# Performance work log

Hardware: AMD Instinct MI355X
Metric: run time of the kernel (lower is better)

The kernel has to match this reference:

```python
import jax, jax.numpy as jnp
import numpy as np

N_NODES = 10000


def gcn_conv(x, W, b, src, dst, num_nodes):
    # PyG GCNConv (eval): h = x @ W; add self-loops; symmetric norm D^-1/2 A D^-1/2; sum-aggregate; + bias
    h = x @ W  # [N, out]
    loop = jnp.arange(num_nodes, dtype=src.dtype)
    s = jnp.concatenate([src, loop])  # [E+N]
    d = jnp.concatenate([dst, loop])
    deg = jax.ops.segment_sum(jnp.ones_like(d, dtype=h.dtype), d, num_segments=num_nodes)
    dinv = jnp.where(deg > 0, jax.lax.rsqrt(deg), 0.0)
    norm = dinv[s] * dinv[d]  # [E+N]
    msg = h[s] * norm[:, None]  # gather + scale
    out = jax.ops.segment_sum(msg, d, num_segments=num_nodes)  # scatter-add to dst
    return out + b


def setup_inputs() -> dict:
    key = jax.random.key(0)
    k1, k2, k3, k4 = jax.random.split(key, 4)
    in_c, hid_c, out_c = 512, 512, 256
    x = jax.random.normal(k1, (N_NODES, in_c), dtype=jnp.float32)
    edge_index = jax.random.randint(k2, (2, 160000), 0, N_NODES, dtype=jnp.int64)
    W1 = jax.random.normal(k3, (in_c, hid_c), dtype=jnp.float32) * (1.0 / np.sqrt(in_c))
    b1 = jnp.zeros((hid_c,), dtype=jnp.float32)
    W2 = jax.random.normal(k4, (hid_c, out_c), dtype=jnp.float32) * (1.0 / np.sqrt(hid_c))
    b2 = jnp.zeros((out_c,), dtype=jnp.float32)
    return {"x": x, "edge_index": edge_index, "W1": W1, "b1": b1, "W2": W2, "b2": b2}


def reference(x, edge_index, W1, b1, W2, b2):
    src, dst = edge_index[0], edge_index[1]
    h = gcn_conv(x, W1, b1, src, dst, N_NODES)
    h = jax.nn.relu(h)
    # dropout(p=0.5) is identity in eval mode
    z = gcn_conv(h, W2, b2, src, dst, N_NODES)
    return z
```

## Files before the change

### kernel.cpp

```cpp
#include <hip/hip_runtime.h>

#define NN   10000

typedef float f32x4 __attribute__((ext_vector_type(4)));
typedef short s16x8 __attribute__((ext_vector_type(8)));
typedef short s16x4 __attribute__((ext_vector_type(4)));

__device__ __forceinline__ unsigned int f2bf(float f) {
  unsigned int u = __float_as_uint(f);
  return (u + 0x7fffu + ((u >> 16) & 1u)) >> 16;
}
__device__ __forceinline__ float bf2f(unsigned int h) {
  return __uint_as_float(h << 16);
}

__global__ void k_zero_int(int* __restrict__ p, int n) {
  int i = blockIdx.x * blockDim.x + threadIdx.x;
  if (i < n) p[i] = 0;
}

__global__ void k_count(const int* __restrict__ dst, int E, int* __restrict__ cnt) {
  int i = blockIdx.x * blockDim.x + threadIdx.x;
  if (i < E) atomicAdd(&cnt[dst[i]], 1);
}

__global__ __launch_bounds__(256) void k_scan(const int* __restrict__ cnt, int n,
                                              int* __restrict__ offs, float* __restrict__ dinv) {
  __shared__ int part[256];
  int t = threadIdx.x;
  int chunk = (n + 255) / 256;
  int lo = t * chunk, hi = min(lo + chunk, n);
  int s = 0;
  for (int i = lo; i < hi; ++i) s += cnt[i];
  part[t] = s;
  __syncthreads();
  for (int d = 1; d < 256; d <<= 1) {
    int v = (t >= d) ? part[t - d] : 0;
    __syncthreads();
    part[t] += v;
    __syncthreads();
  }
  int run = (t == 0) ? 0 : part[t - 1];
  for (int i = lo; i < hi; ++i) {
    offs[i] = run;
    int c = cnt[i];
    run += c;
    dinv[i] = rsqrtf((float)(c + 1));
  }
  if (t == 255) offs[n] = run;
}

__global__ void k_fill(const int* __restrict__ src, const int* __restrict__ dst, int E,
                       const int* __restrict__ offs, int* __restrict__ cur, int* __restrict__ csr) {
  int i = blockIdx.x * blockDim.x + threadIdx.x;
  if (i < E) {
    int d = dst[i];
    int p = atomicAdd(&cur[d], 1);
    csr[offs[d] + p] = src[i];
  }
}

__global__ void k_convw(const float* __restrict__ W, unsigned short* __restrict__ WT, int N) {
  int i = blockIdx.x * blockDim.x + threadIdx.x;
  if (i >= 512 * N) return;
  int k = i / N, n = i - k * N;
  float f = W[i];
  unsigned int hb = f2bf(f);
  WT[(size_t)n * 1024 + k] = (unsigned short)hb;
  WT[(size_t)n * 1024 + 512 + k] = (unsigned short)f2bf(f - bf2f(hb));
}

template <bool ASPLIT>
__global__ __launch_bounds__(256) void k_gemm_mfma(
    const void* __restrict__ Ap, const unsigned short* __restrict__ WT,
    unsigned short* __restrict__ C, int M, int N, int NTN) {
  __shared__ short Wh[64 * 40], Wl[64 * 40], Ahs[64 * 40];
  __shared__ short Als[ASPLIT ? 64 * 40 : 8];

  int nwg = gridDim.x;
  int q = nwg >> 3, r = nwg & 7;
  int xcd = blockIdx.x & 7, idx = blockIdx.x >> 3;
  int swz = (xcd < r ? xcd * (q + 1) : r * (q + 1) + (xcd - r) * q) + idx;
  int bn = (swz % NTN) * 64;
  int bm = (swz / NTN) * 64;

  int t = threadIdx.x;
  int wid = t >> 6, lane = t & 63;
  int wn = wid & 1, wm = wid >> 1;
  int lr = lane & 15, lg = lane >> 4;

  int wrow = t >> 2, kg8 = (t & 3) * 8;
  int arow = t >> 3, kc4 = (t & 7) * 4;
  int brow = t >> 2, kb8 = (t & 3) * 8;

  f32x4 acc[2][2];
  #pragma unroll
  for (int i = 0; i < 2; ++i)
    #pragma unroll
    for (int j = 0; j < 2; ++j) acc[i][j] = (f32x4){0.f, 0.f, 0.f, 0.f};

  const unsigned short* wbase = WT + (size_t)(bn + wrow) * 1024;

  for (int kk = 0; kk < 512; kk += 32) {
    __syncthreads();
    *(s16x8*)&Wh[wrow * 40 + kg8] = *(const s16x8*)&wbase[kk + kg8];
    *(s16x8*)&Wl[wrow * 40 + kg8] = *(const s16x8*)&wbase[512 + kk + kg8];
    if (ASPLIT) {
      const float* A = (const float*)Ap;
      #pragma unroll
      for (int p = 0; p < 2; ++p) {
        int row = arow + p * 32;
        int grow = bm + row;
        float4 v = make_float4(0.f, 0.f, 0.f, 0.f);
        if (grow < M) v = *(const float4*)&A[(size_t)grow * 512 + kk + kc4];
        float fs[4] = {v.x, v.y, v.z, v.w};
        s16x4 hv, lv;
        #pragma unroll
        for (int j = 0; j < 4; ++j) {
          unsigned int hb = f2bf(fs[j]);
          hv[j] = (short)hb;
          lv[j] = (short)f2bf(fs[j] - bf2f(hb));
        }
        *(s16x4*)&Ahs[row * 40 + kc4] = hv;
        *(s16x4*)&Als[row * 40 + kc4] = lv;
      }
    } else {
      const unsigned short* Ab = (const unsigned short*)Ap;
      int grow = bm + brow;
      s16x8 v = (s16x8){0, 0, 0, 0, 0, 0, 0, 0};
      if (grow < M) v = *(const s16x8*)&Ab[(size_t)grow * 512 + kk + kb8];
      *(s16x8*)&Ahs[brow * 40 + kb8] = v;
    }
    __syncthreads();

    s16x8 fwh[2], fwl[2], fah[2], fal[2];
    #pragma unroll
    for (int i = 0; i < 2; ++i) {
      int nr = wn * 32 + i * 16 + lr;
      int mr = wm * 32 + i * 16 + lr;
      fwh[i] = *(const s16x8*)&Wh[nr * 40 + lg * 8];
      fwl[i] = *(const s16x8*)&Wl[nr * 40 + lg * 8];
      fah[i] = *(const s16x8*)&Ahs[mr * 40 + lg * 8];
      if (ASPLIT) fal[i] = *(const s16x8*)&Als[mr * 40 + lg * 8];
    }
    #pragma unroll
    for (int mi = 0; mi < 2; ++mi)
      #pragma unroll
      for (int ni = 0; ni < 2; ++ni) {
        acc[mi][ni] = __builtin_amdgcn_mfma_f32_16x16x32_bf16(fwh[ni], fah[mi], acc[mi][ni], 0, 0, 0);
        acc[mi][ni] = __builtin_amdgcn_mfma_f32_16x16x32_bf16(fwl[ni], fah[mi], acc[mi][ni], 0, 0, 0);
        if (ASPLIT)
          acc[mi][ni] = __builtin_amdgcn_mfma_f32_16x16x32_bf16(fwh[ni], fal[mi], acc[mi][ni], 0, 0, 0);
      }
  }

  #pragma unroll
  for (int mi = 0; mi < 2; ++mi) {
    int m = bm + wm * 32 + mi * 16 + lr;
    if (m < M) {
      #pragma unroll
      for (int ni = 0; ni < 2; ++ni) {
        int n0 = bn + wn * 32 + ni * 16 + lg * 4;
        ushort4 cv;
        cv.x = (unsigned short)f2bf(acc[mi][ni][0]);
        cv.y = (unsigned short)f2bf(acc[mi][ni][1]);
        cv.z = (unsigned short)f2bf(acc[mi][ni][2]);
        cv.w = (unsigned short)f2bf(acc[mi][ni][3]);
        *(ushort4*)&C[(size_t)m * N + n0] = cv;
      }
    }
  }
}

template <int F, bool RELU, bool OUTBF16>
__global__ __launch_bounds__(256) void k_agg_bf(
    const unsigned short* __restrict__ H, const float* __restrict__ dinv,
    const int* __restrict__ offs, const int* __restrict__ csr,
    const float* __restrict__ bias, void* __restrict__ outp) {
  constexpr int FT = F / 8;
  constexpr int EG = 256 / FT;
  __shared__ float red[256][8];
  int node = blockIdx.x;
  int t = threadIdx.x;
  int fc = t % FT;
  int eg = t / FT;
  int lo = offs[node], hi = offs[node + 1];
  float a[8];
  #pragma unroll
  for (int j = 0; j < 8; ++j) a[j] = 0.f;
  for (int e = lo + eg; e < hi; e += EG) {
    int s = csr[e];
    float w = dinv[s];
    s16x8 v = *(const s16x8*)&H[(size_t)s * F + fc * 8];
    #pragma unroll
    for (int j = 0; j < 8; ++j) a[j] += w * bf2f((unsigned short)v[j]);
  }
  #pragma unroll
  for (int j = 0; j < 8; ++j) red[t][j] = a[j];
  __syncthreads();
  if (eg == 0) {
    #pragma unroll
    for (int g = 1; g < EG; ++g)
      #pragma unroll
      for (int j = 0; j < 8; ++j) a[j] += red[g * FT + fc][j];
    float wd = dinv[node];
    s16x8 sv = *(const s16x8*)&H[(size_t)node * F + fc * 8];
    float o[8];
    #pragma unroll
    for (int j = 0; j < 8; ++j) {
      o[j] = wd * (a[j] + wd * bf2f((unsigned short)sv[j])) + bias[fc * 8 + j];
      if (RELU) o[j] = fmaxf(o[j], 0.f);
    }
    if (OUTBF16) {
      s16x8 hv;
      #pragma unroll
      for (int j = 0; j < 8; ++j) hv[j] = (short)f2bf(o[j]);
      *(s16x8*)&((unsigned short*)outp)[(size_t)node * F + fc * 8] = hv;
    } else {
      float* op = (float*)outp;
      *(float4*)&op[(size_t)node * F + fc * 8]     = make_float4(o[0], o[1], o[2], o[3]);
      *(float4*)&op[(size_t)node * F + fc * 8 + 4] = make_float4(o[4], o[5], o[6], o[7]);
    }
  }
}

extern "C" void kernel_launch(void* const* d_in, const int* in_sizes, int n_in,
                              void* d_out, int out_size, void* d_ws, size_t ws_size,
                              hipStream_t stream) {
  (void)n_in; (void)out_size; (void)ws_size;
  const float* x  = (const float*)d_in[0];
  const int*   ei = (const int*)d_in[1];
  const float* W1 = (const float*)d_in[2];
  const float* b1 = (const float*)d_in[3];
  const float* W2 = (const float*)d_in[4];
  const float* b2 = (const float*)d_in[5];
  float* out = (float*)d_out;

  int E = in_sizes[1] / 2;
  const int* src = ei;
  const int* dst = ei + E;

  char* w = (char*)d_ws;
  float*          dinv = (float*)(w);
  int*            cnt  = (int*)(w + 65536);
  int*            cur  = (int*)(w + 131072);
  int*            offs = (int*)(w + 196608);
  int*            csr  = (int*)(w + 262144);
  unsigned short* WT1  = (unsigned short*)(w + 1048576);
  unsigned short* WT2  = (unsigned short*)(w + 2097152);
  unsigned short* h1   = (unsigned short*)(w + 3145728);
  unsigned short* a1   = (unsigned short*)(w + 14680064);
  unsigned short* h2   = (unsigned short*)(w + 26214400);

  k_zero_int<<<(NN + 255) / 256, 256, 0, stream>>>(cnt, NN);
  k_zero_int<<<(NN + 255) / 256, 256, 0, stream>>>(cur, NN);
  k_count<<<(E + 255) / 256, 256, 0, stream>>>(dst, E, cnt);
  k_scan<<<1, 256, 0, stream>>>(cnt, NN, offs, dinv);
  k_fill<<<(E + 255) / 256, 256, 0, stream>>>(src, dst, E, offs, cur, csr);

  k_convw<<<(512 * 512 + 255) / 256, 256, 0, stream>>>(W1, WT1, 512);
  k_convw<<<(512 * 256 + 255) / 256, 256, 0, stream>>>(W2, WT2, 256);

  int ntm = (NN + 63) / 64;
  k_gemm_mfma<true><<<8 * ntm, 256, 0, stream>>>(x, WT1, h1, NN, 512, 8);
  k_agg_bf<512, true, true><<<NN, 256, 0, stream>>>(h1, dinv, offs, csr, b1, a1);
  k_gemm_mfma<false><<<4 * ntm, 256, 0, stream>>>(a1, WT2, h2, NN, 256, 4);
  k_agg_bf<256, false, false><<<NN, 256, 0, stream>>>(h2, dinv, offs, csr, b2, out);
}
```

Baseline: 219.4 us.

## Enlarge GEMM M-tile to 128 rows and merge small setup kernels

The GEMM block tile grows from 64x64 to 128x64, so each wave computes 64 rows with four M fragments and reuses each loaded W fragment across twice as many MFMAs. This halves the number of workgroups and cuts repeated W staging traffic. Separately, the two zeroing kernels and the two weight-conversion kernels are each merged into one launch to save launch overhead. The larger tile raises register and LDS use and leaves fewer blocks, which may lower occupancy.

```diff
diff --git a/kernel.cpp b/kernel.cpp
--- a/kernel.cpp
+++ b/kernel.cpp
@@ -14,9 +14,9 @@
   return __uint_as_float(h << 16);
 }
 
-__global__ void k_zero_int(int* __restrict__ p, int n) {
-  int i = blockIdx.x * blockDim.x + threadIdx.x;
-  if (i < n) p[i] = 0;
+__global__ void k_zero2(int* __restrict__ p0, int* __restrict__ p1, int n) {
+  int i = blockIdx.x * blockDim.x + threadIdx.x;
+  if (i < n) { p0[i] = 0; p1[i] = 0; }
 }
 
 __global__ void k_count(const int* __restrict__ dst, int E, int* __restrict__ cnt) {
@@ -60,29 +60,38 @@
   }
 }
 
-__global__ void k_convw(const float* __restrict__ W, unsigned short* __restrict__ WT, int N) {
-  int i = blockIdx.x * blockDim.x + threadIdx.x;
-  if (i >= 512 * N) return;
-  int k = i / N, n = i - k * N;
-  float f = W[i];
-  unsigned int hb = f2bf(f);
-  WT[(size_t)n * 1024 + k] = (unsigned short)hb;
-  WT[(size_t)n * 1024 + 512 + k] = (unsigned short)f2bf(f - bf2f(hb));
+__global__ void k_convw2(const float* __restrict__ W1, unsigned short* __restrict__ WT1,
+                         const float* __restrict__ W2, unsigned short* __restrict__ WT2) {
+  int i = blockIdx.x * blockDim.x + threadIdx.x;
+  if (i < 512 * 512) {
+    int k = i >> 9, n = i & 511;
+    float f = W1[i];
+    unsigned int hb = f2bf(f);
+    WT1[(size_t)n * 1024 + k] = (unsigned short)hb;
+    WT1[(size_t)n * 1024 + 512 + k] = (unsigned short)f2bf(f - bf2f(hb));
+  } else if (i < 512 * 512 + 512 * 256) {
+    int j = i - 512 * 512;
+    int k = j >> 8, n = j & 255;
+    float f = W2[j];
+    unsigned int hb = f2bf(f);
+    WT2[(size_t)n * 1024 + k] = (unsigned short)hb;
+    WT2[(size_t)n * 1024 + 512 + k] = (unsigned short)f2bf(f - bf2f(hb));
+  }
 }
 
 template <bool ASPLIT>
 __global__ __launch_bounds__(256) void k_gemm_mfma(
     const void* __restrict__ Ap, const unsigned short* __restrict__ WT,
     unsigned short* __restrict__ C, int M, int N, int NTN) {
-  __shared__ short Wh[64 * 40], Wl[64 * 40], Ahs[64 * 40];
-  __shared__ short Als[ASPLIT ? 64 * 40 : 8];
+  __shared__ short Wh[64 * 40], Wl[64 * 40], Ahs[128 * 40];
+  __shared__ short Als[ASPLIT ? 128 * 40 : 8];
 
   int nwg = gridDim.x;
   int q = nwg >> 3, r = nwg & 7;
   int xcd = blockIdx.x & 7, idx = blockIdx.x >> 3;
   int swz = (xcd < r ? xcd * (q + 1) : r * (q + 1) + (xcd - r) * q) + idx;
   int bn = (swz % NTN) * 64;
-  int bm = (swz / NTN) * 64;
+  int bm = (swz / NTN) * 128;
 
   int t = threadIdx.x;
   int wid = t >> 6, lane = t & 63;
@@ -93,9 +102,9 @@
   int arow = t >> 3, kc4 = (t & 7) * 4;
   int brow = t >> 2, kb8 = (t & 3) * 8;
 
-  f32x4 acc[2][2];
-  #pragma unroll
-  for (int i = 0; i < 2; ++i)
+  f32x4 acc[4][2];
+  #pragma unroll
+  for (int i = 0; i < 4; ++i)
     #pragma unroll
     for (int j = 0; j < 2; ++j) acc[i][j] = (f32x4){0.f, 0.f, 0.f, 0.f};
 
@@ -108,7 +117,7 @@
     if (ASPLIT) {
       const float* A = (const float*)Ap;
       #pragma unroll
-      for (int p = 0; p < 2; ++p) {
+      for (int p = 0; p < 4; ++p) {
         int row = arow + p * 32;
         int grow = bm + row;
         float4 v = make_float4(0.f, 0.f, 0.f, 0.f);
@@ -126,25 +135,32 @@
       }
     } else {
       const unsigned short* Ab = (const unsigned short*)Ap;
-      int grow = bm + brow;
-      s16x8 v = (s16x8){0, 0, 0, 0, 0, 0, 0, 0};
-      if (grow < M) v = *(const s16x8*)&Ab[(size_t)grow * 512 + kk + kb8];
-      *(s16x8*)&Ahs[brow * 40 + kb8] = v;
-    }
-    __syncthreads();
-
-    s16x8 fwh[2], fwl[2], fah[2], fal[2];
+      #pragma unroll
+      for (int p = 0; p < 2; ++p) {
+        int row = brow + p * 64;
+        int grow = bm + row;
+        s16x8 v = (s16x8){0, 0, 0, 0, 0, 0, 0, 0};
+        if (grow < M) v = *(const s16x8*)&Ab[(size_t)grow * 512 + kk + kb8];
+        *(s16x8*)&Ahs[row * 40 + kb8] = v;
+      }
+    }
+    __syncthreads();
+
+    s16x8 fwh[2], fwl[2], fah[4], fal[4];
     #pragma unroll
     for (int i = 0; i < 2; ++i) {
       int nr = wn * 32 + i * 16 + lr;
-      int mr = wm * 32 + i * 16 + lr;
       fwh[i] = *(const s16x8*)&Wh[nr * 40 + lg * 8];
       fwl[i] = *(const s16x8*)&Wl[nr * 40 + lg * 8];
+    }
+    #pragma unroll
+    for (int i = 0; i < 4; ++i) {
+      int mr = wm * 64 + i * 16 + lr;
       fah[i] = *(const s16x8*)&Ahs[mr * 40 + lg * 8];
       if (ASPLIT) fal[i] = *(const s16x8*)&Als[mr * 40 + lg * 8];
     }
     #pragma unroll
-    for (int mi = 0; mi < 2; ++mi)
+    for (int mi = 0; mi < 4; ++mi)
       #pragma unroll
       for (int ni = 0; ni < 2; ++ni) {
         acc[mi][ni] = __builtin_amdgcn_mfma_f32_16x16x32_bf16(fwh[ni], fah[mi], acc[mi][ni], 0, 0, 0);
@@ -155,8 +171,8 @@
   }
 
   #pragma unroll
-  for (int mi = 0; mi < 2; ++mi) {
-    int m = bm + wm * 32 + mi * 16 + lr;
+  for (int mi = 0; mi < 4; ++mi) {
+    int m = bm + wm * 64 + mi * 16 + lr;
     if (m < M) {
       #pragma unroll
       for (int ni = 0; ni < 2; ++ni) {
@@ -252,16 +268,13 @@
   unsigned short* a1   = (unsigned short*)(w + 14680064);
   unsigned short* h2   = (unsigned short*)(w + 26214400);
 
-  k_zero_int<<<(NN + 255) / 256, 256, 0, stream>>>(cnt, NN);
-  k_zero_int<<<(NN + 255) / 256, 256, 0, stream>>>(cur, NN);
+  k_zero2<<<(NN + 255) / 256, 256, 0, stream>>>(cnt, cur, NN);
   k_count<<<(E + 255) / 256, 256, 0, stream>>>(dst, E, cnt);
   k_scan<<<1, 256, 0, stream>>>(cnt, NN, offs, dinv);
   k_fill<<<(E + 255) / 256, 256, 0, stream>>>(src, dst, E, offs, cur, csr);
-
-  k_convw<<<(512 * 512 + 255) / 256, 256, 0, stream>>>(W1, WT1, 512);
-  k_convw<<<(512 * 256 + 255) / 256, 256, 0, stream>>>(W2, WT2, 256);
-
-  int ntm = (NN + 63) / 64;
+  k_convw2<<<(512 * 512 + 512 * 256 + 255) / 256, 256, 0, stream>>>(W1, WT1, W2, WT2);
+
+  int ntm = (NN + 127) / 128;
   k_gemm_mfma<true><<<8 * ntm, 256, 0, stream>>>(x, WT1, h1, NN, 512, 8);
   k_agg_bf<512, true, true><<<NN, 256, 0, stream>>>(h1, dinv, offs, csr, b1, a1);
   k_gemm_mfma<false><<<4 * ntm, 256, 0, stream>>>(a1, WT2, h2, NN, 256, 4);
```

Result: slower. 232.5 us (+6.0%).
